# Kernel tuning notes

Measured on AMD Instinct MI355X. Metric: run time of the kernel, lower is better.

The kernel has to match this reference:

```python
import jax, jax.numpy as jnp
import numpy as np

EPS = 1e-5
B, N, NPOINT, K = 16, 4096, 1024, 32
IN_CH, OUT_CH = 64, 64


def index_points(points, idx):
    # points: [B, N, C], idx: [B, ...] -> [B, ..., C]
    b = points.shape[0]
    flat = idx.reshape(b, -1)
    out = jnp.take_along_axis(points, flat[:, :, None], axis=1)
    return out.reshape(idx.shape + (points.shape[-1],))


def bn2d(x, gamma, beta):
    # x: [B, C, H, W], batch-stat BN (training mode), biased variance
    m = x.mean(axis=(0, 2, 3), keepdims=True)
    v = x.var(axis=(0, 2, 3), keepdims=True)
    return gamma[None, :, None, None] * (x - m) / jnp.sqrt(v + EPS) + beta[None, :, None, None]


def bn1d(x, gamma, beta):
    # x: [B, C, L]
    m = x.mean(axis=(0, 2), keepdims=True)
    v = x.var(axis=(0, 2), keepdims=True)
    return gamma[None, :, None] * (x - m) / jnp.sqrt(v + EPS) + beta[None, :, None]


def conv1x1(x, w, b):
    # x: [B, C, H, W], w: [O, C], b: [O]
    return jnp.einsum('bchw,oc->bohw', x, w) + b[None, :, None, None]


def setup_inputs() -> dict:
    key = jax.random.key(0)
    ks = jax.random.split(key, 16)
    inp = {
        'xyz': jax.random.normal(ks[0], (B, N, 3), jnp.float32),
        'points': jax.random.normal(ks[1], (B, N, 61), jnp.float32),
        'local_coordinates': jax.random.normal(ks[2], (B, NPOINT * K, 3), jnp.float32),
        'neighbor_lists': jax.random.randint(ks[3], (B, NPOINT, K), 0, N),
        'data_idx': jax.random.randint(ks[4], (B, NPOINT), 0, N),
        # WeightNet: 3 -> 16 -> 16 -> OUT_CH, each conv1x1 + BN2d + relu
        'w0': jax.random.normal(ks[5], (16, 3), jnp.float32) * 0.1,
        'b0': jnp.zeros((16,), jnp.float32),
        'g0': jnp.ones((16,), jnp.float32),
        'be0': jnp.zeros((16,), jnp.float32),
        'w1': jax.random.normal(ks[6], (16, 16), jnp.float32) * 0.1,
        'b1': jnp.zeros((16,), jnp.float32),
        'g1': jnp.ones((16,), jnp.float32),
        'be1': jnp.zeros((16,), jnp.float32),
        'w2': jax.random.normal(ks[7], (OUT_CH, 16), jnp.float32) * 0.1,
        'b2': jnp.zeros((OUT_CH,), jnp.float32),
        'g2': jnp.ones((OUT_CH,), jnp.float32),
        'be2': jnp.zeros((OUT_CH,), jnp.float32),
        # bn_conv over IN_CH*OUT_CH channels
        'gc': jnp.ones((IN_CH * OUT_CH,), jnp.float32),
        'bc': jnp.zeros((IN_CH * OUT_CH,), jnp.float32),
        # linear IN_CH*OUT_CH -> OUT_CH
        'lw': jax.random.normal(ks[8], (IN_CH * OUT_CH, OUT_CH), jnp.float32) * 0.01,
        'lb': jnp.zeros((OUT_CH,), jnp.float32),
        # bn_linear
        'gl': jnp.ones((OUT_CH,), jnp.float32),
        'bl': jnp.zeros((OUT_CH,), jnp.float32),
    }
    return inp


def reference(xyz, points, local_coordinates, neighbor_lists, data_idx,
              w0, b0, g0, be0, w1, b1, g1, be1, w2, b2, g2, be2,
              gc, bc, lw, lb, gl, bl):
    new_xyz = index_points(xyz, data_idx)                       # [B, NPOINT, 3]
    pts = jnp.concatenate([points, xyz], axis=2)                # [B, N, IN_CH]
    grouped = index_points(pts, neighbor_lists)                 # [B, NPOINT, K, IN_CH]
    grouped = grouped.transpose(0, 1, 3, 2)                     # [B, NPOINT, IN_CH, K]

    # WeightNet on local coordinates
    lc = local_coordinates.reshape(B, NPOINT, K, 3).transpose(0, 3, 2, 1)  # [B, 3, K, NPOINT]
    h = jax.nn.relu(bn2d(conv1x1(lc, w0, b0), g0, be0))
    h = jax.nn.relu(bn2d(conv1x1(h, w1, b1), g1, be1))
    h = jax.nn.relu(bn2d(conv1x1(h, w2, b2), g2, be2))          # [B, OUT_CH, K, NPOINT]
    weights = h.transpose(0, 3, 2, 1)                            # [B, NPOINT, K, OUT_CH]

    # aggregate over neighbors: [B, NPOINT, IN_CH, OUT_CH]
    new_points = jnp.einsum('bnik,bnko->bnio', grouped, weights)
    new_points = new_points.reshape(B, NPOINT, IN_CH * OUT_CH)

    new_points = jax.nn.relu(
        bn1d(new_points.transpose(0, 2, 1), gc, bc).transpose(0, 2, 1))
    new_points = new_points @ lw + lb                            # [B, NPOINT, OUT_CH]
    new_points = bn1d(new_points.transpose(0, 2, 1), gl, bl).transpose(0, 2, 1)
    new_points = jax.nn.relu(new_points)
    return (new_xyz, new_points)
```

## Files before the change

kernel.cpp:

```cpp
#include <hip/hip_runtime.h>
#include <hip/hip_bf16.h>

#define BB 16
#define NN 4096
#define NPOINTS 1024
#define KK 32
#define NPTS (BB*NPOINTS)
#define NWN  (BB*NPOINTS*KK)
#define EPSF 1e-5f
#define SGBLK 512
#define SGIT  4

typedef unsigned short u16;
typedef u16  u16x8 __attribute__((ext_vector_type(8)));
typedef u16  u16x4 __attribute__((ext_vector_type(4)));
typedef short s16x8 __attribute__((ext_vector_type(8)));
typedef float f32x4 __attribute__((ext_vector_type(4)));
typedef float f32x4u __attribute__((ext_vector_type(4), aligned(4)));

__device__ __forceinline__ float bf(u16 u){
  union { unsigned int i; float f; } v; v.i = ((unsigned int)u) << 16; return v.f;
}
__device__ __forceinline__ u16 f2b(float f){
  __hip_bfloat16 h = __float2bfloat16(f);
  union { __hip_bfloat16 hh; u16 u; } v; v.hh = h; return v.u;
}


__global__ __launch_bounds__(256) void k_init(const float* xyz, const int* didx, float* out,
                                              const float* lw, u16* lwbt,
                                              const float* points, u16* ptsw){
  int t = threadIdx.x;
  if (blockIdx.x < 64){
    int p = blockIdx.x * 256 + t;
    int b = p >> 10;
    int idx = didx[p];
    const float* src = xyz + ((size_t)(b * NN + idx)) * 3;
    float* dst = out + (size_t)p * 3;
    dst[0] = src[0]; dst[1] = src[1]; dst[2] = src[2];
  } else if (blockIdx.x < 128){
    __shared__ float T[64][65];
    int ib = blockIdx.x - 64;
    int kb = ib * 64;
    {
      int k = t >> 2, c4 = t & 3;
      #pragma unroll
      for (int j = 0; j < 4; ++j)
        *(f32x4*)&T[k][c4*16 + j*4] = *(const f32x4*)(lw + (size_t)(kb + k)*64 + c4*16 + j*4);
    }
    __syncthreads();
    {
      int n = t >> 2, k4 = t & 3;
      #pragma unroll
      for (int j = 0; j < 16; ++j){
        int k = k4*16 + j;
        lwbt[(size_t)n*4096 + k*64 + ib] = f2b(T[k][n]);
      }
    }
  } else {
    int gid0 = (blockIdx.x - 128) * 256 + t;
    #pragma unroll
    for (int rep = 0; rep < 4; ++rep){
      int idx = gid0 + rep * 131072;
      int row = idx >> 3, c8 = idx & 7;
      const float* prow = points + (size_t)row * 61;
      u16x8 g;
      if (c8 < 7){
        f32x4 lo = *(const f32x4u*)(prow + c8*8);
        f32x4 hi = *(const f32x4u*)(prow + c8*8 + 4);
        g[0]=f2b(lo.x); g[1]=f2b(lo.y); g[2]=f2b(lo.z); g[3]=f2b(lo.w);
        g[4]=f2b(hi.x); g[5]=f2b(hi.y); g[6]=f2b(hi.z); g[7]=f2b(hi.w);
      } else {
        const float* xr = xyz + (size_t)row * 3;
        f32x4 lo = *(const f32x4u*)(prow + 56);
        g[0]=f2b(lo.x); g[1]=f2b(lo.y); g[2]=f2b(lo.z); g[3]=f2b(lo.w);
        g[4]=f2b(prow[60]);
        g[5]=f2b(xr[0]); g[6]=f2b(xr[1]); g[7]=f2b(xr[2]);
      }
      *(u16x8*)(ptsw + (size_t)row*64 + c8*8) = g;
    }
  }
}

__global__ __launch_bounds__(256) void k_stat0(const float* lc, float* PA){
  int t = threadIdx.x;
  float a[9];
  #pragma unroll
  for (int r = 0; r < 9; ++r) a[r] = 0.f;
  size_t base = (size_t)blockIdx.x * 1024 + t;
  for (int ip = 0; ip < 4; ++ip){
    size_t p = base + (size_t)ip * 256;
    float x0 = lc[p*3], x1 = lc[p*3+1], x2 = lc[p*3+2];
    a[0]+=x0; a[1]+=x1; a[2]+=x2;
    a[3]+=x0*x0; a[4]+=x0*x1; a[5]+=x0*x2;
    a[6]+=x1*x1; a[7]+=x1*x2; a[8]+=x2*x2;
  }
  #pragma unroll
  for (int m = 1; m < 64; m <<= 1){
    #pragma unroll
    for (int r = 0; r < 9; ++r) a[r] += __shfl_xor(a[r], m);
  }
  if ((t & 63) == 0){
    float* dst = PA + (size_t)(blockIdx.x*4 + (t>>6)) * 16;
    f32x4 v0 = {a[0],a[1],a[2],a[3]}, v1 = {a[4],a[5],a[6],a[7]}, v2 = {a[8],0.f,0.f,0.f};
    *(f32x4*)dst = v0; *(f32x4*)(dst+4) = v1; *(f32x4*)(dst+8) = v2;
  }
}

__global__ __launch_bounds__(256) void k_red0(const float* PA, const float* w0, const float* b0,
                                              const float* g0, const float* be0, float* F){
  __shared__ float ms[12];
  __shared__ float a0sh[16];
  int t = threadIdx.x;
  if (t < 12){
    float s0=0,s1=0,s2=0,s3=0;
    const float* p = PA + t;
    for (int r = 0; r < 2048; r += 4){
      s0 += p[(size_t)(r+0)*16]; s1 += p[(size_t)(r+1)*16];
      s2 += p[(size_t)(r+2)*16]; s3 += p[(size_t)(r+3)*16];
    }
    ms[t] = (s0+s1)+(s2+s3);
  }
  __syncthreads();
  if (t < 16){
    float wx = w0[t*3], wy = w0[t*3+1], wz = w0[t*3+2], bb = b0[t];
    float lin = wx*ms[0] + wy*ms[1] + wz*ms[2];
    float quad = wx*wx*ms[3] + wy*wy*ms[6] + wz*wz*ms[8]
               + 2.f*(wx*wy*ms[4] + wx*wz*ms[5] + wy*wz*ms[7]);
    float S = lin + (float)NWN * bb;
    float Q = quad + 2.f*bb*lin + (float)NWN*bb*bb;
    float m = S * (1.f/NWN);
    float v = Q * (1.f/NWN) - m*m;
    float a = g0[t] * rsqrtf(v + EPSF);
    float d = be0[t] - m*a;
    a0sh[t] = a;
    F[48+t] = a*bb + d;
  }
  __syncthreads();
  if (t < 48) F[t] = a0sh[t/3] * w0[t];
}

template<bool L2>
__global__ __launch_bounds__(256) void k_statG(const float* lc, const float* F, float* PB){
  __shared__ f32x4 w0p[16];
  __shared__ float w1s[256], b1fs[16];
  __shared__ __align__(16) u16 Ht[4][16*72];
  __shared__ float GS[4][16][17];
  __shared__ float SHs[4][16];
  int t = threadIdx.x;
  int w = t >> 6, l = t & 63;
  if (t < 16){
    f32x4 wv = {F[t*3], F[t*3+1], F[t*3+2], F[48+t]};
    w0p[t] = wv;
    if (L2) b1fs[t] = F[320+t];
  }
  if (L2) w1s[t] = F[64+t];
  __syncthreads();
  f32x4 acc = {0.f,0.f,0.f,0.f};
  float sh[16];
  #pragma unroll
  for (int r = 0; r < 16; ++r) sh[r] = 0.f;
  u16* Hw = &Ht[w][0];
  for (int it = 0; it < SGIT; ++it){
    size_t p = (size_t)blockIdx.x * (SGIT*256) + (size_t)it*256 + w*64 + l;
    float x0 = lc[p*3], x1 = lc[p*3+1], x2 = lc[p*3+2];
    float h[16];
    #pragma unroll
    for (int oc = 0; oc < 16; ++oc){
      f32x4 wv = w0p[oc];
      h[oc] = fmaxf(0.f, wv.x*x0 + wv.y*x1 + wv.z*x2 + wv.w);
    }
    if (L2){
      float h1[16];
      #pragma unroll
      for (int oc = 0; oc < 16; ++oc){
        const f32x4* wr = (const f32x4*)&w1s[oc*16];
        f32x4 wa = wr[0], wb = wr[1], wc = wr[2], wd = wr[3];
        float y = b1fs[oc];
        y += wa.x*h[0]  + wa.y*h[1]  + wa.z*h[2]  + wa.w*h[3];
        y += wb.x*h[4]  + wb.y*h[5]  + wb.z*h[6]  + wb.w*h[7];
        y += wc.x*h[8]  + wc.y*h[9]  + wc.z*h[10] + wc.w*h[11];
        y += wd.x*h[12] + wd.y*h[13] + wd.z*h[14] + wd.w*h[15];
        h1[oc] = fmaxf(0.f, y);
      }
      #pragma unroll
      for (int oc = 0; oc < 16; ++oc) h[oc] = h1[oc];
    }
    #pragma unroll
    for (int oc = 0; oc < 16; ++oc) sh[oc] += h[oc];
    #pragma unroll
    for (int c = 0; c < 16; ++c) Hw[c*72 + l] = f2b(h[c]);
    __syncthreads();
    #pragma unroll
    for (int tt = 0; tt < 2; ++tt){
      s16x8 af = *(const s16x8*)&Hw[(l & 15)*72 + tt*32 + (l >> 4)*8];
      acc = __builtin_amdgcn_mfma_f32_16x16x32_bf16(af, af, acc, 0, 0, 0);
    }
    __syncthreads();
  }
  #pragma unroll
  for (int r = 0; r < 4; ++r)
    GS[w][(l>>4)*4 + r][l & 15] = acc[r];
  #pragma unroll
  for (int m = 1; m < 64; m <<= 1){
    #pragma unroll
    for (int r = 0; r < 16; ++r) sh[r] += __shfl_xor(sh[r], m);
  }
  if (l == 0){
    #pragma unroll
    for (int r = 0; r < 16; ++r) SHs[w][r] = sh[r];
  }
  __syncthreads();
  {
    int i = t >> 4, j = t & 15;
    float g = GS[0][i][j] + GS[1][i][j] + GS[2][i][j] + GS[3][i][j];
    PB[(size_t)blockIdx.x*272 + t] = g;
    if (t < 16)
      PB[(size_t)blockIdx.x*272 + 256 + t] = SHs[0][t]+SHs[1][t]+SHs[2][t]+SHs[3][t];
  }
}

__global__ __launch_bounds__(256) void k_red1(const float* PB, const float* w1, const float* b1,
                                              const float* g1, const float* be1, float* F,
                                              u16* w1Bg){
  __shared__ float red[272];
  __shared__ float a1sh[16];
  int t = threadIdx.x;
  for (int e = t; e < 272; e += 256){
    float s = 0.f;
    for (int r = 0; r < SGBLK; ++r) s += PB[(size_t)r*272 + e];
    red[e] = s;
  }
  __syncthreads();
  if (t < 16){
    float wv[16];
    #pragma unroll
    for (int ic = 0; ic < 16; ++ic) wv[ic] = w1[t*16+ic];
    float lin = 0.f;
    #pragma unroll
    for (int ic = 0; ic < 16; ++ic) lin += wv[ic]*red[256+ic];
    float quad = 0.f;
    for (int i = 0; i < 16; ++i){
      float ri = 0.f;
      #pragma unroll
      for (int j = 0; j < 16; ++j) ri += wv[j]*red[i*16+j];
      quad += wv[i]*ri;
    }
    float bb = b1[t];
    float S = lin + (float)NWN * bb;
    float Q = quad + 2.f*bb*lin + (float)NWN*bb*bb;
    float m = S * (1.f/NWN);
    float v = Q * (1.f/NWN) - m*m;
    float a = g1[t] * rsqrtf(v + EPSF);
    float d = be1[t] - m*a;
    a1sh[t] = a;
    F[320+t] = a*bb + d;
  }
  __syncthreads();
  F[64 + t] = a1sh[t >> 4] * w1[t];
  if (t < 64){
    int oc = t & 15, icb = (t >> 4) * 8;
    u16x8 fr;
    #pragma unroll
    for (int j = 0; j < 8; ++j){
      int ic = icb + j;
      fr[j] = (ic < 16) ? f2b(a1sh[oc] * w1[oc*16 + ic]) : (u16)0;
    }
    *(u16x8*)&w1Bg[t*8] = fr;
  }
}

__global__ __launch_bounds__(256) void k_red2(const float* PB, const float* w2, const float* b2,
                                              const float* g2, const float* be2, float* F,
                                              u16* w2Bg){
  __shared__ float red[272];
  __shared__ float a2sh[64];
  int t = threadIdx.x;
  for (int e = t; e < 272; e += 256){
    float s = 0.f;
    for (int r = 0; r < SGBLK; ++r) s += PB[(size_t)r*272 + e];
    red[e] = s;
  }
  __syncthreads();
  if (t < 64){
    float wv[16];
    #pragma unroll
    for (int ic = 0; ic < 16; ++ic) wv[ic] = w2[t*16+ic];
    float lin = 0.f;
    #pragma unroll
    for (int ic = 0; ic < 16; ++ic) lin += wv[ic]*red[256+ic];
    float quad = 0.f;
    for (int i = 0; i < 16; ++i){
      float ri = 0.f;
      #pragma unroll
      for (int j = 0; j < 16; ++j) ri += wv[j]*red[i*16+j];
      quad += wv[i]*ri;
    }
    float bb = b2[t];
    float S = lin + (float)NWN * bb;
    float Q = quad + 2.f*bb*lin + (float)NWN*bb*bb;
    float m = S * (1.f/NWN);
    float v = Q * (1.f/NWN) - m*m;
    float a = g2[t] * rsqrtf(v + EPSF);
    float d = be2[t] - m*a;
    a2sh[t] = a;
    F[1360+t] = a*bb + d;
  }
  __syncthreads();
  for (int i = t; i < 1024; i += 256) F[336+i] = a2sh[i >> 4] * w2[i];
  {
    int ot = t >> 6, lane = t & 63;
    int oc = ot*16 + (lane & 15), icb = ((lane >> 4)) * 8;
    u16x8 fr;
    #pragma unroll
    for (int j = 0; j < 8; ++j){
      int ic = icb + j;
      fr[j] = (ic < 16) ? f2b(a2sh[oc] * w2[oc*16 + ic]) : (u16)0;
    }
    *(u16x8*)&w2Bg[t*8] = fr;
  }
}

__global__ __launch_bounds__(256) void k_main(const float* lcg, const int* nbrg,
    const u16* ptsw, const float* F,
    const u16* w1Bg, const u16* w2Bg,
    u16* npw){
  __shared__ __align__(16) u16 Gr[64*40];
  __shared__ __align__(16) u16 Wr[64*40];
  __shared__ __align__(16) u16 H0bf[32*40];
  __shared__ __align__(16) u16 H1bf[32*40];
  __shared__ float w0c[48], b0c[16];
  int t = threadIdx.x;
  int w = t >> 6, l = t & 63;
  int point = blockIdx.x;
  int bb = point >> 10;
  s16x8 w1B = *(const s16x8*)&w1Bg[l*8];
  int otA = (w & 1)*2, otB = otA + 1;
  s16x8 w2BA = *(const s16x8*)&w2Bg[(otA*64 + l)*8];
  s16x8 w2BB = *(const s16x8*)&w2Bg[(otB*64 + l)*8];
  float b1f = F[320 + (l & 15)];
  float b2fA = F[1360 + otA*16 + (l & 15)];
  float b2fB = F[1360 + otB*16 + (l & 15)];
  if (t < 48) w0c[t] = F[t];
  if (t < 16) b0c[t] = F[48+t];
  {
    int k = t >> 3, c = 16 + (t & 7)*2;
    *(unsigned int*)&H0bf[k*40 + c] = 0u;
    *(unsigned int*)&H1bf[k*40 + c] = 0u;
  }
  {
    int kg = w*8 + (l >> 3), c8 = l & 7;
    int n = nbrg[(size_t)point*32 + kg];
    u16x8 g = *(const u16x8*)(ptsw + (size_t)(bb * NN + n)*64 + c8*8);
    #pragma unroll
    for (int j = 0; j < 8; ++j)
      Gr[(c8*8 + j)*40 + kg] = g[j];
  }
  __syncthreads();
  {
    int k = t >> 3, oc0 = (t & 7)*2;
    const float* xp = lcg + (size_t)point*96 + k*3;
    float x0 = xp[0], x1 = xp[1], x2 = xp[2];
    #pragma unroll
    for (int e = 0; e < 2; ++e){
      int oc = oc0 + e;
      float y = w0c[oc*3]*x0 + w0c[oc*3+1]*x1 + w0c[oc*3+2]*x2 + b0c[oc];
      H0bf[k*40 + oc] = f2b(fmaxf(0.f, y));
    }
  }
  __syncthreads();
  if (w < 2){
    int kt = w;
    s16x8 af = *(const s16x8*)&H0bf[(kt*16 + (l & 15))*40 + (l >> 4)*8];
    f32x4 acc = {b1f, b1f, b1f, b1f};
    acc = __builtin_amdgcn_mfma_f32_16x16x32_bf16(af, w1B, acc, 0, 0, 0);
    #pragma unroll
    for (int r = 0; r < 4; ++r)
      H1bf[(kt*16 + (l >> 4)*4 + r)*40 + (l & 15)] = f2b(fmaxf(0.f, acc[r]));
  }
  __syncthreads();
  {
    int kt = w >> 1;
    s16x8 af = *(const s16x8*)&H1bf[(kt*16 + (l & 15))*40 + (l >> 4)*8];
    int kbase = kt*16 + (l >> 4)*4;
    f32x4 accA = {b2fA, b2fA, b2fA, b2fA};
    accA = __builtin_amdgcn_mfma_f32_16x16x32_bf16(af, w2BA, accA, 0, 0, 0);
    u16x4 sA;
    sA[0]=f2b(fmaxf(0.f,accA[0])); sA[1]=f2b(fmaxf(0.f,accA[1]));
    sA[2]=f2b(fmaxf(0.f,accA[2])); sA[3]=f2b(fmaxf(0.f,accA[3]));
    *(u16x4*)&Wr[(otA*16 + (l & 15))*40 + kbase] = sA;
    f32x4 accB = {b2fB, b2fB, b2fB, b2fB};
    accB = __builtin_amdgcn_mfma_f32_16x16x32_bf16(af, w2BB, accB, 0, 0, 0);
    u16x4 sB;
    sB[0]=f2b(fmaxf(0.f,accB[0])); sB[1]=f2b(fmaxf(0.f,accB[1]));
    sB[2]=f2b(fmaxf(0.f,accB[2])); sB[3]=f2b(fmaxf(0.f,accB[3]));
    *(u16x4*)&Wr[(otB*16 + (l & 15))*40 + kbase] = sB;
  }
  __syncthreads();
  {
    int li = l & 15, lk = (l >> 4) * 8, lr = (l >> 4) * 4;
    s16x8 bfrag = *(const s16x8*)&Wr[(w*16 + li)*40 + lk];
    size_t obase = (size_t)point*4096 + (size_t)(w*16 + li)*64 + lr;
    #pragma unroll
    for (int it = 0; it < 4; ++it){
      s16x8 afrag = *(const s16x8*)&Gr[(it*16 + li)*40 + lk];
      f32x4 z = {0.f, 0.f, 0.f, 0.f};
      f32x4 d = __builtin_amdgcn_mfma_f32_16x16x32_bf16(afrag, bfrag, z, 0, 0, 0);
      u16x4 st;
      st[0] = f2b(d[0]); st[1] = f2b(d[1]); st[2] = f2b(d[2]); st[3] = f2b(d[3]);
      *(u16x4*)(npw + obase + it*16) = st;
    }
  }
}

__global__ __launch_bounds__(256) void k_statC(const u16* npw, float* PC){
  int t = threadIdx.x;
  float s[16], q[16];
  #pragma unroll
  for (int j = 0; j < 16; ++j){ s[j] = 0.f; q[j] = 0.f; }
  size_t rowbase = (size_t)blockIdx.x * 64;
  for (int p = 0; p < 64; ++p){
    const u16* row = npw + (rowbase + p) * 4096 + t * 16;
    u16x8 a = *(const u16x8*)row;
    u16x8 b = *(const u16x8*)(row + 8);
    #pragma unroll
    for (int j = 0; j < 8; ++j){ float v = bf(a[j]); s[j]   += v; q[j]   += v*v; }
    #pragma unroll
    for (int j = 0; j < 8; ++j){ float v = bf(b[j]); s[8+j] += v; q[8+j] += v*v; }
  }
  float* dst = PC + (size_t)blockIdx.x * 8192 + t * 16;
  #pragma unroll
  for (int j = 0; j < 16; ++j){ dst[j] = s[j]; dst[4096 + j] = q[j]; }
}

__global__ __launch_bounds__(256) void k_finC(const float* PC, const float* gc, const float* bc,
                                              float* AC, float* DC){
  int qpos = blockIdx.x * 256 + threadIdx.x;
  float s = 0.f, q = 0.f;
  for (int r = 0; r < 256; ++r){
    s += PC[(size_t)r * 8192 + qpos];
    q += PC[(size_t)r * 8192 + 4096 + qpos];
  }
  int ch = (qpos & 63)*64 + (qpos >> 6);
  float m = s * (1.f/16384.f);
  float v = q * (1.f/16384.f) - m*m;
  float a = gc[ch] * rsqrtf(v + EPSF);
  AC[qpos] = a; DC[qpos] = bc[ch] - m*a;
}

__global__ __launch_bounds__(256) void k_linear(const u16* npw, const float* AC, const float* DC,
                                                const u16* lwbt, const float* lb, float* yw,
                                                float* PL){
  __shared__ u16 Al[32*72];
  __shared__ u16 Bl[64*72];
  __shared__ float cps[64], cpq[64];
  int t = threadIdx.x;
  int w = t >> 6, l = t & 63;
  int rowbase = blockIdx.x * 32;
  int mt = w & 1, np2 = w >> 1;
  f32x4 acc0 = {0.f,0.f,0.f,0.f}, acc1 = acc0;
  for (int kb = 0; kb < 4096; kb += 64){
    __syncthreads();
    {
      int r = t >> 3, c8 = t & 7;
      int kk = kb + c8*8;
      u16x8 u = *(const u16x8*)(npw + (size_t)(rowbase + r)*4096 + kk);
      f32x4 alo = *(const f32x4*)(AC + kk), ahi = *(const f32x4*)(AC + kk + 4);
      f32x4 dlo = *(const f32x4*)(DC + kk), dhi = *(const f32x4*)(DC + kk + 4);
      u16x8 o;
      o[0] = f2b(fmaxf(0.f, alo.x*bf(u[0]) + dlo.x));
      o[1] = f2b(fmaxf(0.f, alo.y*bf(u[1]) + dlo.y));
      o[2] = f2b(fmaxf(0.f, alo.z*bf(u[2]) + dlo.z));
      o[3] = f2b(fmaxf(0.f, alo.w*bf(u[3]) + dlo.w));
      o[4] = f2b(fmaxf(0.f, ahi.x*bf(u[4]) + dhi.x));
      o[5] = f2b(fmaxf(0.f, ahi.y*bf(u[5]) + dhi.y));
      o[6] = f2b(fmaxf(0.f, ahi.z*bf(u[6]) + dhi.z));
      o[7] = f2b(fmaxf(0.f, ahi.w*bf(u[7]) + dhi.w));
      *(u16x8*)&Al[r*72 + c8*8] = o;
    }
    #pragma unroll
    for (int jj = 0; jj < 2; ++jj){
      int n = (t >> 3) + jj*32, c8 = t & 7;
      u16x8 u = *(const u16x8*)(lwbt + (size_t)n*4096 + kb + c8*8);
      *(u16x8*)&Bl[n*72 + c8*8] = u;
    }
    __syncthreads();
    #pragma unroll
    for (int ks = 0; ks < 2; ++ks){
      s16x8 af  = *(const s16x8*)&Al[(mt*16 + (l & 15))*72 + ks*32 + (l >> 4)*8];
      s16x8 bf0 = *(const s16x8*)&Bl[((np2*2    )*16 + (l & 15))*72 + ks*32 + (l >> 4)*8];
      s16x8 bf1 = *(const s16x8*)&Bl[((np2*2 + 1)*16 + (l & 15))*72 + ks*32 + (l >> 4)*8];
      acc0 = __builtin_amdgcn_mfma_f32_16x16x32_bf16(af, bf0, acc0, 0, 0, 0);
      acc1 = __builtin_amdgcn_mfma_f32_16x16x32_bf16(af, bf1, acc1, 0, 0, 0);
    }
  }
  int col0 = np2*32 + (l & 15), col1 = col0 + 16;
  float lb0 = lb[col0], lb1 = lb[col1];
  float s0 = 0.f, q0 = 0.f, s1 = 0.f, q1 = 0.f;
  if (t < 64){ cps[t] = 0.f; cpq[t] = 0.f; }
  __syncthreads();
  #pragma unroll
  for (int r = 0; r < 4; ++r){
    int row = rowbase + mt*16 + (l >> 4)*4 + r;
    float y0 = acc0[r] + lb0;
    float y1 = acc1[r] + lb1;
    yw[(size_t)row*64 + col0] = y0;
    yw[(size_t)row*64 + col1] = y1;
    s0 += y0; q0 += y0*y0; s1 += y1; q1 += y1*y1;
  }
  atomicAdd(&cps[col0], s0); atomicAdd(&cpq[col0], q0);
  atomicAdd(&cps[col1], s1); atomicAdd(&cpq[col1], q1);
  __syncthreads();
  if (t < 64){
    PL[blockIdx.x*128 + t]      = cps[t];
    PL[blockIdx.x*128 + 64 + t] = cpq[t];
  }
}

__global__ __launch_bounds__(128) void k_redF(const float* PL, float* SL){
  int t = threadIdx.x;
  float s = 0.f;
  for (int b = 0; b < 512; ++b) s += PL[b*128 + t];
  SL[t] = s;
}

__global__ __launch_bounds__(256) void k_final(const float* yw, const float* SL,
                                               const float* gl, const float* bl, float* out){
  int e = (blockIdx.x * 256 + threadIdx.x) * 4;
  int o = e & 63;
  f32x4 y = *(const f32x4*)(yw + e);
  f32x4 r;
  #pragma unroll
  for (int j = 0; j < 4; ++j){
    float m = SL[o+j] * (1.f/16384.f);
    float v = SL[64+o+j] * (1.f/16384.f) - m*m;
    float a = gl[o+j] * rsqrtf(v + EPSF);
    float d = bl[o+j] - m*a;
    r[j] = fmaxf(0.f, a*y[j] + d);
  }
  *(f32x4*)(out + 49152 + e) = r;
}

extern "C" void kernel_launch(void* const* d_in, const int* in_sizes, int n_in,
                              void* d_out, int out_size, void* d_ws, size_t ws_size,
                              hipStream_t stream){
  (void)in_sizes; (void)n_in; (void)out_size; (void)ws_size;
  const float* xyz    = (const float*)d_in[0];
  const float* points = (const float*)d_in[1];
  const float* lc     = (const float*)d_in[2];
  const int*   nbrl   = (const int*)d_in[3];
  const int*   didx   = (const int*)d_in[4];
  const float* w0 = (const float*)d_in[5];
  const float* b0 = (const float*)d_in[6];
  const float* g0 = (const float*)d_in[7];
  const float* be0= (const float*)d_in[8];
  const float* w1 = (const float*)d_in[9];
  const float* b1 = (const float*)d_in[10];
  const float* g1 = (const float*)d_in[11];
  const float* be1= (const float*)d_in[12];
  const float* w2 = (const float*)d_in[13];
  const float* b2 = (const float*)d_in[14];
  const float* g2 = (const float*)d_in[15];
  const float* be2= (const float*)d_in[16];
  const float* gc = (const float*)d_in[17];
  const float* bc = (const float*)d_in[18];
  const float* lw = (const float*)d_in[19];
  const float* lb = (const float*)d_in[20];
  const float* gl = (const float*)d_in[21];
  const float* bl = (const float*)d_in[22];
  float* out = (float*)d_out;
  char* ws = (char*)d_ws;

  float* F   = (float*)ws;
  float* SL  = F + 1536;
  float* AC  = SL + 128;
  float* DC  = AC + 4096;
  float* PA  = DC + 4096;
  float* PB1 = PA + 32768;
  float* PB2 = PB1 + 139264;
  float* PL  = PB2 + 139264;
  u16*  w1Bg = (u16*)(PL + 65536);
  u16*  w2Bg = w1Bg + 512;
  float* PC  = (float*)(ws + 4194304);
  u16*  npw  = (u16*)(ws + 4194304 + 8388608);
  float* yw  = (float*)(ws + 4194304 + 8388608 + 134217728);
  u16*  lwbt = (u16*)(ws + 4194304 + 8388608 + 134217728 + 4194304);
  u16*  ptsw = (u16*)(ws + 4194304 + 8388608 + 134217728 + 4194304 + 1048576);

  k_init  <<<640,   256, 0, stream>>>(xyz, didx, out, lw, lwbt, points, ptsw);
  k_stat0 <<<512,   256, 0, stream>>>(lc, PA);
  k_red0  <<<1,     256, 0, stream>>>(PA, w0, b0, g0, be0, F);
  k_statG<false><<<SGBLK, 256, 0, stream>>>(lc, F, PB1);
  k_red1  <<<1,     256, 0, stream>>>(PB1, w1, b1, g1, be1, F, w1Bg);
  k_statG<true> <<<SGBLK, 256, 0, stream>>>(lc, F, PB2);
  k_red2  <<<1,     256, 0, stream>>>(PB2, w2, b2, g2, be2, F, w2Bg);
  k_main  <<<16384, 256, 0, stream>>>(lc, nbrl, ptsw, F, w1Bg, w2Bg, npw);
  k_statC <<<256,   256, 0, stream>>>(npw, PC);
  k_finC  <<<16,    256, 0, stream>>>(PC, gc, bc, AC, DC);
  k_linear<<<512,   256, 0, stream>>>(npw, AC, DC, lwbt, lb, yw, PL);
  k_redF  <<<1,     128, 0, stream>>>(PL, SL);
  k_final <<<1024,  256, 0, stream>>>(yw, SL, gl, bl, out);
}
```

Before: 266.7 us.

## Use MFMA for layer-1 in second stat pass and swizzle gather LDS

The second WeightNet statistics pass used to compute the 16x16 layer-1 product with scalar FMAs. It now stages bf16 layer-0 activations in LDS and runs them through MFMA with the prepacked w1 fragment, so it matches the bf16 path used by the main kernel. Separately, the gathered neighbour tile in the main kernel gets an XOR swizzle on the k index to reduce LDS bank conflicts on scatter and fragment reads. The first change shifts the statistics from fp32 to bf16 layer-1 values and adds an extra barrier and LDS round trip per iteration.

```diff
diff --git a/kernel.cpp b/kernel.cpp
--- a/kernel.cpp
+++ b/kernel.cpp
@@ -140,10 +140,8 @@
   if (t < 48) F[t] = a0sh[t/3] * w0[t];
 }
 
-template<bool L2>
-__global__ __launch_bounds__(256) void k_statG(const float* lc, const float* F, float* PB){
+__global__ __launch_bounds__(256) void k_statG1(const float* lc, const float* F, float* PB){
   __shared__ f32x4 w0p[16];
-  __shared__ float w1s[256], b1fs[16];
   __shared__ __align__(16) u16 Ht[4][16*72];
   __shared__ float GS[4][16][17];
   __shared__ float SHs[4][16];
@@ -152,9 +150,7 @@
   if (t < 16){
     f32x4 wv = {F[t*3], F[t*3+1], F[t*3+2], F[48+t]};
     w0p[t] = wv;
-    if (L2) b1fs[t] = F[320+t];
-  }
-  if (L2) w1s[t] = F[64+t];
+  }
   __syncthreads();
   f32x4 acc = {0.f,0.f,0.f,0.f};
   float sh[16];
@@ -169,25 +165,8 @@
     for (int oc = 0; oc < 16; ++oc){
       f32x4 wv = w0p[oc];
       h[oc] = fmaxf(0.f, wv.x*x0 + wv.y*x1 + wv.z*x2 + wv.w);
-    }
-    if (L2){
-      float h1[16];
-      #pragma unroll
-      for (int oc = 0; oc < 16; ++oc){
-        const f32x4* wr = (const f32x4*)&w1s[oc*16];
-        f32x4 wa = wr[0], wb = wr[1], wc = wr[2], wd = wr[3];
-        float y = b1fs[oc];
-        y += wa.x*h[0]  + wa.y*h[1]  + wa.z*h[2]  + wa.w*h[3];
-        y += wb.x*h[4]  + wb.y*h[5]  + wb.z*h[6]  + wb.w*h[7];
-        y += wc.x*h[8]  + wc.y*h[9]  + wc.z*h[10] + wc.w*h[11];
-        y += wd.x*h[12] + wd.y*h[13] + wd.z*h[14] + wd.w*h[15];
-        h1[oc] = fmaxf(0.f, y);
-      }
-      #pragma unroll
-      for (int oc = 0; oc < 16; ++oc) h[oc] = h1[oc];
-    }
-    #pragma unroll
-    for (int oc = 0; oc < 16; ++oc) sh[oc] += h[oc];
+      sh[oc] += h[oc];
+    }
     #pragma unroll
     for (int c = 0; c < 16; ++c) Hw[c*72 + l] = f2b(h[c]);
     __syncthreads();
@@ -210,6 +189,84 @@
     #pragma unroll
     for (int r = 0; r < 16; ++r) SHs[w][r] = sh[r];
   }
+  __syncthreads();
+  {
+    int i = t >> 4, j = t & 15;
+    float g = GS[0][i][j] + GS[1][i][j] + GS[2][i][j] + GS[3][i][j];
+    PB[(size_t)blockIdx.x*272 + t] = g;
+    if (t < 16)
+      PB[(size_t)blockIdx.x*272 + 256 + t] = SHs[0][t]+SHs[1][t]+SHs[2][t]+SHs[3][t];
+  }
+}
+
+__global__ __launch_bounds__(256) void k_statG2(const float* lc, const float* F,
+                                                const u16* w1Bg, float* PB){
+  __shared__ f32x4 w0p[16];
+  __shared__ __align__(16) u16 Ht0[4][64*40];
+  __shared__ __align__(16) u16 Ht1[4][16*72];
+  __shared__ float GS[4][16][17];
+  __shared__ float SHs[4][16];
+  int t = threadIdx.x;
+  int w = t >> 6, l = t & 63;
+  if (t < 16){
+    f32x4 wv = {F[t*3], F[t*3+1], F[t*3+2], F[48+t]};
+    w0p[t] = wv;
+  }
+  s16x8 w1B = *(const s16x8*)&w1Bg[l*8];
+  float b1f = F[320 + (l & 15)];
+  u16* H0w = &Ht0[w][0];
+  u16* H1w = &Ht1[w][0];
+  {
+    u16x8 z8 = {0,0,0,0,0,0,0,0};
+    *(u16x8*)&H0w[l*40 + 16] = z8;
+    *(u16x8*)&H0w[l*40 + 24] = z8;
+  }
+  __syncthreads();
+  f32x4 acc = {0.f,0.f,0.f,0.f};
+  float shloc = 0.f;
+  for (int it = 0; it < SGIT; ++it){
+    size_t p = (size_t)blockIdx.x * (SGIT*256) + (size_t)it*256 + w*64 + l;
+    float x0 = lc[p*3], x1 = lc[p*3+1], x2 = lc[p*3+2];
+    u16x8 p0, p1;
+    #pragma unroll
+    for (int oc = 0; oc < 8; ++oc){
+      f32x4 wv = w0p[oc];
+      p0[oc] = f2b(fmaxf(0.f, wv.x*x0 + wv.y*x1 + wv.z*x2 + wv.w));
+    }
+    #pragma unroll
+    for (int oc = 0; oc < 8; ++oc){
+      f32x4 wv = w0p[8+oc];
+      p1[oc] = f2b(fmaxf(0.f, wv.x*x0 + wv.y*x1 + wv.z*x2 + wv.w));
+    }
+    *(u16x8*)&H0w[l*40]     = p0;
+    *(u16x8*)&H0w[l*40 + 8] = p1;
+    __syncthreads();
+    #pragma unroll
+    for (int mt = 0; mt < 4; ++mt){
+      s16x8 af = *(const s16x8*)&H0w[(mt*16 + (l & 15))*40 + (l >> 4)*8];
+      f32x4 c = {b1f, b1f, b1f, b1f};
+      c = __builtin_amdgcn_mfma_f32_16x16x32_bf16(af, w1B, c, 0, 0, 0);
+      #pragma unroll
+      for (int r = 0; r < 4; ++r){
+        float v = fmaxf(0.f, c[r]);
+        shloc += v;
+        H1w[(l & 15)*72 + mt*16 + (l >> 4)*4 + r] = f2b(v);
+      }
+    }
+    __syncthreads();
+    #pragma unroll
+    for (int tt = 0; tt < 2; ++tt){
+      s16x8 afg = *(const s16x8*)&H1w[(l & 15)*72 + tt*32 + (l >> 4)*8];
+      acc = __builtin_amdgcn_mfma_f32_16x16x32_bf16(afg, afg, acc, 0, 0, 0);
+    }
+    __syncthreads();
+  }
+  #pragma unroll
+  for (int r = 0; r < 4; ++r)
+    GS[w][(l>>4)*4 + r][l & 15] = acc[r];
+  shloc += __shfl_xor(shloc, 16);
+  shloc += __shfl_xor(shloc, 32);
+  if (l < 16) SHs[w][l] = shloc;
   __syncthreads();
   {
     int i = t >> 4, j = t & 15;
@@ -352,9 +409,10 @@
     int kg = w*8 + (l >> 3), c8 = l & 7;
     int n = nbrg[(size_t)point*32 + kg];
     u16x8 g = *(const u16x8*)(ptsw + (size_t)(bb * NN + n)*64 + c8*8);
+    int kphys = ((w ^ (c8 & 3)) << 3) + (l >> 3);
     #pragma unroll
     for (int j = 0; j < 8; ++j)
-      Gr[(c8*8 + j)*40 + kg] = g[j];
+      Gr[(c8*8 + j)*40 + kphys] = g[j];
   }
   __syncthreads();
   {
@@ -398,12 +456,14 @@
   }
   __syncthreads();
   {
-    int li = l & 15, lk = (l >> 4) * 8, lr = (l >> 4) * 4;
-    s16x8 bfrag = *(const s16x8*)&Wr[(w*16 + li)*40 + lk];
+    int li = l & 15, lkb = l >> 4, lr = (l >> 4) * 4;
+    s16x8 bfrag = *(const s16x8*)&Wr[(w*16 + li)*40 + lkb*8];
     size_t obase = (size_t)point*4096 + (size_t)(w*16 + li)*64 + lr;
     #pragma unroll
     for (int it = 0; it < 4; ++it){
-      s16x8 afrag = *(const s16x8*)&Gr[(it*16 + li)*40 + lk];
+      int ch = it*16 + li;
+      int key = (ch >> 3) & 3;
+      s16x8 afrag = *(const s16x8*)&Gr[ch*40 + ((lkb ^ key) << 3)];
       f32x4 z = {0.f, 0.f, 0.f, 0.f};
       f32x4 d = __builtin_amdgcn_mfma_f32_16x16x32_bf16(afrag, bfrag, z, 0, 0, 0);
       u16x4 st;
@@ -590,9 +650,9 @@
   k_init  <<<640,   256, 0, stream>>>(xyz, didx, out, lw, lwbt, points, ptsw);
   k_stat0 <<<512,   256, 0, stream>>>(lc, PA);
   k_red0  <<<1,     256, 0, stream>>>(PA, w0, b0, g0, be0, F);
-  k_statG<false><<<SGBLK, 256, 0, stream>>>(lc, F, PB1);
+  k_statG1<<<SGBLK, 256, 0, stream>>>(lc, F, PB1);
   k_red1  <<<1,     256, 0, stream>>>(PB1, w1, b1, g1, be1, F, w1Bg);
-  k_statG<true> <<<SGBLK, 256, 0, stream>>>(lc, F, PB2);
+  k_statG2<<<SGBLK, 256, 0, stream>>>(lc, F, w1Bg, PB2);
   k_red2  <<<1,     256, 0, stream>>>(PB2, w2, b2, g2, be2, F, w2Bg);
   k_main  <<<16384, 256, 0, stream>>>(lc, nbrl, ptsw, F, w1Bg, w2Bg, npw);
   k_statC <<<256,   256, 0, stream>>>(npw, PC);
```

After: 258.7 us. -3.0%, faster.
